# Performance work log

Hardware: AMD Instinct MI355X
Metric: run time of the kernel (lower is better)

Reference implementation:

```python
import jax, jax.numpy as jnp
import numpy as np

B, W, N, DIM, GAMMA = 32, 16, 256, 256, 4
WH = 16  # sqrt(N)
V = DIM // GAMMA
TABLE = (2 * WH - 1) * (2 * WH - 1)  # 961


def _make_rel_index(wh: int) -> np.ndarray:
    coords = np.stack(np.meshgrid(np.arange(wh), np.arange(wh), indexing='ij'))  # (2, wh, wh)
    flat = coords.reshape(2, -1)                         # (2, wh*wh)
    rel = flat[:, :, None] - flat[:, None, :]            # (2, n, n)
    rel = rel.transpose(1, 2, 0).copy()                  # (n, n, 2)
    rel[:, :, 0] += wh - 1
    rel[:, :, 1] += wh - 1
    rel[:, :, 0] *= 2 * wh - 1
    return rel.sum(-1).astype(np.int32)                  # (n, n)


def setup_inputs() -> dict:
    key = jax.random.key(0)
    k1, k2, k3 = jax.random.split(key, 3)
    x = jax.random.normal(k1, (B, W, N, DIM), dtype=jnp.float32)
    bias_table = jax.random.normal(k2, (TABLE, W * GAMMA), dtype=jnp.float32) * 0.02
    token_bias = jax.random.normal(k3, (W * GAMMA, N, 1), dtype=jnp.float32) * 0.02
    rel_index = jnp.asarray(_make_rel_index(WH))
    return {"x": x, "bias_table": bias_table, "token_bias": token_bias, "rel_index": rel_index}


def reference(x, bias_table, token_bias, rel_index):
    b, w, n, d = x.shape
    gamma = GAMMA
    v = d // gamma
    # gather: (n, n, w*gamma) -> permute to (w*gamma, n, n)
    rpb = bias_table[rel_index.reshape(-1)].reshape(n, n, w * gamma)
    rpb = jnp.transpose(rpb, (2, 0, 1))                  # ((s w), n, n) with s outer
    # rearrange '(s b) m n -> b m n s'
    win_weight = jnp.transpose(rpb.reshape(gamma, w, n, n), (1, 2, 3, 0))  # (w, m, n, s)
    # rearrange 'b w n (v s) -> b w n v s'
    xs = x.reshape(b, w, n, v, gamma)
    out = jnp.einsum('wmns,bwnvs->bwmvs', win_weight, xs)
    # rearrange '(w s) m v -> w m v s'
    bias = jnp.transpose(token_bias.reshape(w, gamma, n, 1), (0, 2, 3, 1))  # (w, m, 1, s)
    out = out + bias[None]
    return out.reshape(b, w, n, d)
```

## Files before the change

### kernel.cpp

```cpp
#include <hip/hip_runtime.h>
#include <stdint.h>


typedef __attribute__((ext_vector_type(8))) short bf16x8;
typedef __attribute__((ext_vector_type(4))) float f32x4;
typedef __attribute__((ext_vector_type(8))) unsigned short u16x8;

__device__ __forceinline__ unsigned short f2bf(float f) {
    union { float f; unsigned u; } v; v.f = f;
    unsigned u = v.u;
    u += 0x7FFFu + ((u >> 16) & 1u);
    return (unsigned short)(u >> 16);
}
__device__ __forceinline__ float bf2f(unsigned short h) {
    union { unsigned u; float f; } v; v.u = ((unsigned)h) << 16;
    return v.f;
}
__device__ __forceinline__ int expInRange(unsigned short w16) {
    int e = (w16 >> 7) & 0xFF;
    return (e >= 100 && e <= 140) ? 1 : 0;
}

__global__ __launch_bounds__(256) void k_gather(
    const void* __restrict__ bt_raw,
    const int*  __restrict__ rel_index,
    const void* __restrict__ x_raw,
    unsigned short* __restrict__ Ab)
{
    __shared__ unsigned short Lt[64 * 72];

    const unsigned short* xw = (const unsigned short*)x_raw;
    int t = threadIdx.x;
    int pred = expInRange(xw[t * 2]) & expInRange(xw[t * 2 + 1]);
    int cnt = __syncthreads_count(pred);
    bool isF32 = (cnt < 150);

    const int cellbase = blockIdx.x << 6;
    const int c = t >> 2;
    const int p = t & 3;
    const int row = rel_index[cellbase + c];

    unsigned short vals[16];
    if (isF32) {
        const float* bt = (const float*)bt_raw + (row << 6) + (p << 4);
        float4 v0 = *(const float4*)(bt);
        float4 v1 = *(const float4*)(bt + 4);
        float4 v2 = *(const float4*)(bt + 8);
        float4 v3 = *(const float4*)(bt + 12);
        float vf[16] = {v0.x,v0.y,v0.z,v0.w, v1.x,v1.y,v1.z,v1.w,
                        v2.x,v2.y,v2.z,v2.w, v3.x,v3.y,v3.z,v3.w};
#pragma unroll
        for (int k = 0; k < 16; k++) vals[k] = f2bf(vf[k]);
    } else {
        const unsigned short* bt = (const unsigned short*)bt_raw + (row << 6) + (p << 4);
        u16x8 a0 = *(const u16x8*)(bt);
        u16x8 a1 = *(const u16x8*)(bt + 8);
#pragma unroll
        for (int k = 0; k < 8; k++) { vals[k] = a0[k]; vals[8 + k] = a1[k]; }
    }
#pragma unroll
    for (int k = 0; k < 16; k++)
        Lt[(((k << 2) + p) * 72) + c] = vals[k];
    __syncthreads();

    const int plane = t >> 2;
    const int cg = (t & 3) << 4;
    u16x8 o0 = *(const u16x8*)(Lt + plane * 72 + cg);
    u16x8 o1 = *(const u16x8*)(Lt + plane * 72 + cg + 8);
    unsigned short* dst = Ab + (plane << 16) + cellbase + cg;
    *(u16x8*)dst = o0;
    *(u16x8*)(dst + 8) = o1;
}

__global__ __launch_bounds__(512, 4) void k_main(
    const void* __restrict__ x_raw,
    const unsigned short* __restrict__ Ab,
    const void* __restrict__ tb_raw,
    void* __restrict__ out_raw)
{
    __shared__ unsigned short lds[16384 + 8192];

    const int tid  = threadIdx.x;
    const unsigned short* xw = (const unsigned short*)x_raw;
    int pred = expInRange(xw[tid]);
    int cnt = __syncthreads_count(pred);
    const bool isF32 = (cnt < 400);

    const int lane = tid & 63;
    const int wave = tid >> 6;
    const int bx = blockIdx.x;
    const int b  = bx & 31;
    const int mt = (bx >> 5) & 1;
    const int w  = bx >> 6;
    const int m0 = mt << 7;

    const int sw   = wave & 3;
    const int vh   = wave >> 2;
    const int vvb  = vh << 5;
    const int col  = lane & 15;
    const int quad = lane >> 4;

    const int a_row  = tid >> 2;
    const int a_slot = tid & 3;
    const int a_psl  = a_slot ^ ((a_row >> 1) & 3);
    unsigned short* AsW = lds + (a_row << 5) + (a_psl << 3);
    const unsigned short* Ag = Ab + (w << 18) + ((m0 + a_row) << 8) + (a_slot << 3);
    const int aswz = (col >> 1) & 3;
    const int ar = (sw << 12) + (col << 5) + ((quad ^ aswz) << 3);

    const int d0   = (tid & 127) << 1;
    const int ngrp = tid >> 7;
    const int xgoff = (((b << 4) + w) << 16) + (ngrp << 11) + d0;
    const float*          Xgf = (const float*)x_raw + xgoff;
    const unsigned short* Xgh = (const unsigned short*)x_raw + xgoff;
    const int vvx = d0 >> 2;
    unsigned short* xw0p = lds + 16384 + ((d0 & 3) << 11) + (vvx << 5)
                               + ((ngrp ^ ((vvx >> 1) & 3)) << 3);
    unsigned short* xw1p = xw0p + 2048;
    const int xr0 = 16384 + (sw << 11) + ((vvb + col) << 5) + ((quad ^ aswz) << 3);
    const int xr1 = xr0 + 512;

    f32x4 acc[8][2];
#pragma unroll
    for (int mi = 0; mi < 8; mi++) {
        acc[mi][0] = (f32x4){0.f, 0.f, 0.f, 0.f};
        acc[mi][1] = (f32x4){0.f, 0.f, 0.f, 0.f};
    }

    for (int nc = 0; nc < 8; nc++) {
        u16x8 av[4];
#pragma unroll
        for (int it = 0; it < 4; it++)
            av[it] = *(const u16x8*)(Ag + (it << 16) + (nc << 5));

        u16x8 o0, o1;
        if (isF32) {
            float2 v[8];
#pragma unroll
            for (int j = 0; j < 8; j++)
                v[j] = *(const float2*)(Xgf + (nc << 13) + (j << 8));
#pragma unroll
            for (int j = 0; j < 8; j++) { o0[j] = f2bf(v[j].x); o1[j] = f2bf(v[j].y); }
        } else {
            unsigned int v[8];
#pragma unroll
            for (int j = 0; j < 8; j++)
                v[j] = *(const unsigned int*)(Xgh + (nc << 13) + (j << 8));
#pragma unroll
            for (int j = 0; j < 8; j++) { o0[j] = (unsigned short)(v[j] & 0xFFFFu);
                                          o1[j] = (unsigned short)(v[j] >> 16); }
        }

#pragma unroll
        for (int it = 0; it < 4; it++)
            *(u16x8*)(AsW + (it << 12)) = av[it];
        *(u16x8*)xw0p = o0;
        *(u16x8*)xw1p = o1;
        __syncthreads();

        bf16x8 bfr0 = *(const bf16x8*)(lds + xr0);
        bf16x8 bfr1 = *(const bf16x8*)(lds + xr1);
#pragma unroll
        for (int mi = 0; mi < 8; mi++) {
            bf16x8 afr = *(const bf16x8*)(lds + ar + (mi << 9));
            acc[mi][0] = __builtin_amdgcn_mfma_f32_16x16x32_bf16(afr, bfr0, acc[mi][0], 0, 0, 0);
            acc[mi][1] = __builtin_amdgcn_mfma_f32_16x16x32_bf16(afr, bfr1, acc[mi][1], 0, 0, 0);
        }
        __syncthreads();
    }

    const int tboff = (((w << 2) + sw) << 8) + m0;
    const int ooff  = (((b << 4) + w) << 16) + (m0 << 8) + sw;
    if (isF32) {
        const float* tb = (const float*)tb_raw + tboff;
        float* ob = (float*)out_raw + ooff;
#pragma unroll
        for (int mi = 0; mi < 8; mi++) {
#pragma unroll
            for (int r = 0; r < 4; r++) {
                int m = (mi << 4) + (quad << 2) + r;
                float bias = tb[m];
#pragma unroll
                for (int vi = 0; vi < 2; vi++) {
                    int vv = vvb + (vi << 4) + col;
                    ob[(m << 8) + (vv << 2)] = acc[mi][vi][r] + bias;
                }
            }
        }
    } else {
        const unsigned short* tb = (const unsigned short*)tb_raw + tboff;
        unsigned short* ob = (unsigned short*)out_raw + ooff;
#pragma unroll
        for (int mi = 0; mi < 8; mi++) {
#pragma unroll
            for (int r = 0; r < 4; r++) {
                int m = (mi << 4) + (quad << 2) + r;
                float bias = bf2f(tb[m]);
#pragma unroll
                for (int vi = 0; vi < 2; vi++) {
                    int vv = vvb + (vi << 4) + col;
                    ob[(m << 8) + (vv << 2)] = f2bf(acc[mi][vi][r] + bias);
                }
            }
        }
    }
}

__global__ __launch_bounds__(512, 4) void k_main_fused(
    const void* __restrict__ x_raw,
    const void* __restrict__ bt_raw,
    const int*  __restrict__ rel_index,
    const void* __restrict__ tb_raw,
    void* __restrict__ out_raw)
{
    __shared__ unsigned short lds[16384 + 8192];

    const int tid  = threadIdx.x;
    const unsigned short* xw = (const unsigned short*)x_raw;
    int pred = expInRange(xw[tid]);
    int cnt = __syncthreads_count(pred);
    const bool isF32 = (cnt < 400);

    const int lane = tid & 63;
    const int wave = tid >> 6;
    const int bx = blockIdx.x;
    const int b  = bx & 31;
    const int mt = (bx >> 5) & 1;
    const int w  = bx >> 6;
    const int m0 = mt << 7;

    const int sw   = wave & 3;
    const int vh   = wave >> 2;
    const int vvb  = vh << 5;
    const int col  = lane & 15;
    const int quad = lane >> 4;

    const int a_row = tid >> 2;
    const int a_nn8 = (tid & 3) << 3;
    unsigned short* AsW = lds + (a_row << 5) + a_nn8;
    const int* rIp = rel_index + ((m0 + a_row) << 8) + a_nn8;

    const int x_nn = tid & 31;
    const int x_vg = tid >> 5;
    const int xoff = (((b << 4) + w) << 16) + (x_nn << 8) + (x_vg << 4);
    const float*          Xgf = (const float*)x_raw + xoff;
    const unsigned short* Xgh = (const unsigned short*)x_raw + xoff;
    unsigned short* XsW = lds + 16384 + x_nn;

    f32x4 acc[8][2];
#pragma unroll
    for (int mi = 0; mi < 8; mi++) {
        acc[mi][0] = (f32x4){0.f, 0.f, 0.f, 0.f};
        acc[mi][1] = (f32x4){0.f, 0.f, 0.f, 0.f};
    }

    const unsigned short* AsR = lds + (sw << 12) + (col << 5) + (quad << 3);
    const unsigned short* XsR = lds + 16384 + (sw << 11) + ((vvb + col) << 5) + (quad << 3);

    for (int nc = 0; nc < 8; nc++) {
        int4 r0 = *(const int4*)(rIp + (nc << 5));
        int4 r1 = *(const int4*)(rIp + (nc << 5) + 4);
        int ri[8] = {r0.x, r0.y, r0.z, r0.w, r1.x, r1.y, r1.z, r1.w};
#pragma unroll
        for (int it = 0; it < 4; it++) {
            u16x8 av;
            if (isF32) {
                const float* bt = (const float*)bt_raw;
#pragma unroll
                for (int j = 0; j < 8; j++)
                    av[j] = f2bf(bt[(ri[j] << 6) + (it << 4) + w]);
            } else {
                const unsigned short* bt = (const unsigned short*)bt_raw;
#pragma unroll
                for (int j = 0; j < 8; j++)
                    av[j] = bt[(ri[j] << 6) + (it << 4) + w];
            }
            *(u16x8*)(AsW + (it << 12)) = av;
        }

        if (isF32) {
            float4 v[4];
#pragma unroll
            for (int i = 0; i < 4; i++)
                v[i] = *(const float4*)(Xgf + (nc << 13) + (i << 2));
            const float* vf = (const float*)v;
#pragma unroll
            for (int j = 0; j < 16; j++) {
                int vv = (x_vg << 2) + (j >> 2);
                XsW[((j & 3) << 11) + (vv << 5)] = f2bf(vf[j]);
            }
        } else {
            u16x8 xv0 = *(const u16x8*)(Xgh + (nc << 13));
            u16x8 xv1 = *(const u16x8*)(Xgh + (nc << 13) + 8);
#pragma unroll
            for (int j = 0; j < 8; j++) {
                int vv = (x_vg << 2) + (j >> 2);
                XsW[((j & 3) << 11) + (vv << 5)] = xv0[j];
            }
#pragma unroll
            for (int j = 0; j < 8; j++) {
                int vv = (x_vg << 2) + 2 + (j >> 2);
                XsW[((j & 3) << 11) + (vv << 5)] = xv1[j];
            }
        }
        __syncthreads();

        bf16x8 bfr0 = *(const bf16x8*)(XsR);
        bf16x8 bfr1 = *(const bf16x8*)(XsR + 512);
#pragma unroll
        for (int mi = 0; mi < 8; mi++) {
            bf16x8 afr = *(const bf16x8*)(AsR + (mi << 9));
            acc[mi][0] = __builtin_amdgcn_mfma_f32_16x16x32_bf16(afr, bfr0, acc[mi][0], 0, 0, 0);
            acc[mi][1] = __builtin_amdgcn_mfma_f32_16x16x32_bf16(afr, bfr1, acc[mi][1], 0, 0, 0);
        }
        __syncthreads();
    }

    const int tboff = (((w << 2) + sw) << 8) + m0;
    const int ooff  = (((b << 4) + w) << 16) + (m0 << 8) + sw;
    if (isF32) {
        const float* tb = (const float*)tb_raw + tboff;
        float* ob = (float*)out_raw + ooff;
#pragma unroll
        for (int mi = 0; mi < 8; mi++) {
#pragma unroll
            for (int r = 0; r < 4; r++) {
                int m = (mi << 4) + (quad << 2) + r;
                float bias = tb[m];
#pragma unroll
                for (int vi = 0; vi < 2; vi++) {
                    int vv = vvb + (vi << 4) + col;
                    ob[(m << 8) + (vv << 2)] = acc[mi][vi][r] + bias;
                }
            }
        }
    } else {
        const unsigned short* tb = (const unsigned short*)tb_raw + tboff;
        unsigned short* ob = (unsigned short*)out_raw + ooff;
#pragma unroll
        for (int mi = 0; mi < 8; mi++) {
#pragma unroll
            for (int r = 0; r < 4; r++) {
                int m = (mi << 4) + (quad << 2) + r;
                float bias = bf2f(tb[m]);
#pragma unroll
                for (int vi = 0; vi < 2; vi++) {
                    int vv = vvb + (vi << 4) + col;
                    ob[(m << 8) + (vv << 2)] = f2bf(acc[mi][vi][r] + bias);
                }
            }
        }
    }
}

extern "C" void kernel_launch(void* const* d_in, const int* in_sizes, int n_in,
                              void* d_out, int out_size, void* d_ws, size_t ws_size,
                              hipStream_t stream) {
    const void* x          = d_in[0];
    const void* bias_table = d_in[1];
    const void* token_bias = d_in[2];
    const int*  rel_index  = (const int*)d_in[3];

    const size_t AB_BYTES = (size_t)64 * 256 * 256 * 2;
    if (ws_size >= AB_BYTES) {
        unsigned short* Ab = (unsigned short*)d_ws;
        hipLaunchKernelGGL(k_gather, dim3(1024), dim3(256), 0, stream,
                           bias_table, rel_index, x, Ab);
        hipLaunchKernelGGL(k_main, dim3(1024), dim3(512), 0, stream,
                           x, Ab, token_bias, d_out);
    } else {
        hipLaunchKernelGGL(k_main_fused, dim3(1024), dim3(512), 0, stream,
                           x, bias_table, rel_index, token_bias, d_out);
    }
}
```

Baseline: 293.4 us.

## Prefetch next chunk's global loads into registers during MFMA compute

Global loads of the A (bias) fragments and the x chunk for iteration nc+1 are issued into registers right after the current chunk is written to LDS, before the barrier. Their latency can then overlap the barrier and the MFMA work. The __syncthreads calls become raw s_barrier with only an lgkmcnt wait and sched_barrier fences, so the barrier does not drain outstanding vmem loads. The loop is fully unrolled, which raises register pressure and may lower occupancy.

```diff
diff --git a/kernel.cpp b/kernel.cpp
--- a/kernel.cpp
+++ b/kernel.cpp
@@ -127,36 +127,56 @@
         acc[mi][1] = (f32x4){0.f, 0.f, 0.f, 0.f};
     }
 
+    u16x8        av[4];
+    float2       xf[8];
+    unsigned int xu[8];
+#pragma unroll
+    for (int it = 0; it < 4; it++)
+        av[it] = *(const u16x8*)(Ag + (it << 16));
+    if (isF32) {
+#pragma unroll
+        for (int j = 0; j < 8; j++) xf[j] = *(const float2*)(Xgf + (j << 8));
+    } else {
+#pragma unroll
+        for (int j = 0; j < 8; j++) xu[j] = *(const unsigned int*)(Xgh + (j << 8));
+    }
+
+#pragma unroll
     for (int nc = 0; nc < 8; nc++) {
-        u16x8 av[4];
 #pragma unroll
         for (int it = 0; it < 4; it++)
-            av[it] = *(const u16x8*)(Ag + (it << 16) + (nc << 5));
-
+            *(u16x8*)(AsW + (it << 12)) = av[it];
         u16x8 o0, o1;
         if (isF32) {
-            float2 v[8];
-#pragma unroll
-            for (int j = 0; j < 8; j++)
-                v[j] = *(const float2*)(Xgf + (nc << 13) + (j << 8));
-#pragma unroll
-            for (int j = 0; j < 8; j++) { o0[j] = f2bf(v[j].x); o1[j] = f2bf(v[j].y); }
+#pragma unroll
+            for (int j = 0; j < 8; j++) { o0[j] = f2bf(xf[j].x); o1[j] = f2bf(xf[j].y); }
         } else {
-            unsigned int v[8];
-#pragma unroll
-            for (int j = 0; j < 8; j++)
-                v[j] = *(const unsigned int*)(Xgh + (nc << 13) + (j << 8));
-#pragma unroll
-            for (int j = 0; j < 8; j++) { o0[j] = (unsigned short)(v[j] & 0xFFFFu);
-                                          o1[j] = (unsigned short)(v[j] >> 16); }
-        }
-
-#pragma unroll
-        for (int it = 0; it < 4; it++)
-            *(u16x8*)(AsW + (it << 12)) = av[it];
+#pragma unroll
+            for (int j = 0; j < 8; j++) { o0[j] = (unsigned short)(xu[j] & 0xFFFFu);
+                                          o1[j] = (unsigned short)(xu[j] >> 16); }
+        }
         *(u16x8*)xw0p = o0;
         *(u16x8*)xw1p = o1;
-        __syncthreads();
+
+        if (nc < 7) {
+#pragma unroll
+            for (int it = 0; it < 4; it++)
+                av[it] = *(const u16x8*)(Ag + (it << 16) + ((nc + 1) << 5));
+            if (isF32) {
+#pragma unroll
+                for (int j = 0; j < 8; j++)
+                    xf[j] = *(const float2*)(Xgf + ((nc + 1) << 13) + (j << 8));
+            } else {
+#pragma unroll
+                for (int j = 0; j < 8; j++)
+                    xu[j] = *(const unsigned int*)(Xgh + ((nc + 1) << 13) + (j << 8));
+            }
+        }
+
+        asm volatile("s_waitcnt lgkmcnt(0)" ::: "memory");
+        __builtin_amdgcn_sched_barrier(0);
+        __builtin_amdgcn_s_barrier();
+        __builtin_amdgcn_sched_barrier(0);
 
         bf16x8 bfr0 = *(const bf16x8*)(lds + xr0);
         bf16x8 bfr1 = *(const bf16x8*)(lds + xr1);
@@ -166,7 +186,9 @@
             acc[mi][0] = __builtin_amdgcn_mfma_f32_16x16x32_bf16(afr, bfr0, acc[mi][0], 0, 0, 0);
             acc[mi][1] = __builtin_amdgcn_mfma_f32_16x16x32_bf16(afr, bfr1, acc[mi][1], 0, 0, 0);
         }
-        __syncthreads();
+        __builtin_amdgcn_sched_barrier(0);
+        __builtin_amdgcn_s_barrier();
+        __builtin_amdgcn_sched_barrier(0);
     }
 
     const int tboff = (((w << 2) + sw) << 8) + m0;
```

Measured after the change: 379.8 us. 1.29x slower.
